# Kernel tuning notes

Hardware: AMD Instinct MI355X
Metric: run time of the kernel (lower is better)

Reference implementation:

```python
import jax, jax.numpy as jnp
import numpy as np

NUM_BINS = 64
BIN_WIDTH = 0.0625
X_SHAPE = (64, 4, 512, 512)  # SD-style latent batch, ~268 MB fp32


def setup_inputs() -> dict:
    key = jax.random.key(0)
    x = jax.random.normal(key, X_SHAPE, dtype=jnp.float32)
    # uniform bin centers over [-2, 2), step = BIN_WIDTH (matches init_kwargs)
    bins = (-2.0 + BIN_WIDTH * jnp.arange(NUM_BINS)).astype(jnp.float32)
    bin_width = jnp.float32(BIN_WIDTH)
    return {"x": x, "bins": bins, "bin_width": bin_width}


def reference(x, bins, bin_width):
    # out[b] = mean(0.5 - 0.5 * tanh((x - bins[b]) / bin_width * 2))
    # lax.map over the small fixed bin axis avoids materializing a
    # [num_bins, *x.shape] intermediate, matching the original's per-bin
    # streaming reduction.
    scale = 2.0 / bin_width

    def per_bin(c):
        return jnp.mean(0.5 - 0.5 * jnp.tanh((x - c) * scale))

    return jax.lax.map(per_bin, bins)  # shape [NUM_BINS]
```

## Files before the change

kernel.cpp:

```cpp
#include <hip/hip_runtime.h>
#include <hip/hip_bf16.h>


#define NCELLS (74 * 64)
#define HIST_BLOCKS 1024
#define HIST_THREADS 256

__global__ void __launch_bounds__(HIST_THREADS)
hist_kernel(const float* __restrict__ x, unsigned* __restrict__ ghist, int n)
{
    __shared__ unsigned hist[NCELLS];
    for (int i = threadIdx.x; i < NCELLS; i += HIST_THREADS) hist[i] = 0u;
    __syncthreads();

    const int n4 = n >> 2;
    const float4* __restrict__ x4 = (const float4*)x;
    const int gid    = blockIdx.x * HIST_THREADS + threadIdx.x;
    const int stride = gridDim.x * HIST_THREADS;

    for (int i = gid; i < n4; i += stride) {
        float4 v = x4[i];
        {
            int f = (int)floorf(fmaf(v.x, 1024.0f, 2368.0f));
            f = min(max(f, 0), NCELLS - 1);
            atomicAdd(&hist[f], 1u);
        }
        {
            int f = (int)floorf(fmaf(v.y, 1024.0f, 2368.0f));
            f = min(max(f, 0), NCELLS - 1);
            atomicAdd(&hist[f], 1u);
        }
        {
            int f = (int)floorf(fmaf(v.z, 1024.0f, 2368.0f));
            f = min(max(f, 0), NCELLS - 1);
            atomicAdd(&hist[f], 1u);
        }
        {
            int f = (int)floorf(fmaf(v.w, 1024.0f, 2368.0f));
            f = min(max(f, 0), NCELLS - 1);
            atomicAdd(&hist[f], 1u);
        }
    }

    if (blockIdx.x == 0) {
        int tail = n & 3;
        if (threadIdx.x < tail) {
            float v = x[n4 * 4 + threadIdx.x];
            int f = (int)floorf(fmaf(v, 1024.0f, 2368.0f));
            f = min(max(f, 0), NCELLS - 1);
            atomicAdd(&hist[f], 1u);
        }
    }

    __syncthreads();
    for (int i = threadIdx.x; i < NCELLS; i += HIST_THREADS) {
        unsigned v = hist[i];
        if (v) atomicAdd(&ghist[i], v);
    }
}

__global__ void __launch_bounds__(256)
bins_kernel(const unsigned* __restrict__ ghist, float* __restrict__ out, float invN)
{
    const int b = blockIdx.x;
    double sum = 0.0;
    for (int f = threadIdx.x; f < NCELLS; f += 256) {
        unsigned h = ghist[f];
        if (h) {
            float t = -5.0f + ((float)f + 0.5f) * (1.0f / 64.0f);
            float z = 4.0f * ((float)b - t);
            float s = 1.0f / (1.0f + __expf(-z));
            sum += (double)h * (double)s;
        }
    }
    __shared__ double sd[256];
    sd[threadIdx.x] = sum;
    __syncthreads();
    for (int ofs = 128; ofs > 0; ofs >>= 1) {
        if (threadIdx.x < ofs) sd[threadIdx.x] += sd[threadIdx.x + ofs];
        __syncthreads();
    }
    if (threadIdx.x == 0) out[b] = (float)(sd[0] * (double)invN);
}

extern "C" void kernel_launch(void* const* d_in, const int* in_sizes, int n_in,
                              void* d_out, int out_size, void* d_ws, size_t ws_size,
                              hipStream_t stream)
{
    const float* x = (const float*)d_in[0];
    const int n = in_sizes[0];
    unsigned* ghist = (unsigned*)d_ws;

    hipMemsetAsync(d_ws, 0, NCELLS * sizeof(unsigned), stream);

    hist_kernel<<<HIST_BLOCKS, HIST_THREADS, 0, stream>>>(x, ghist, n);
    bins_kernel<<<64, 256, 0, stream>>>(ghist, (float*)d_out, 1.0f / (float)n);
}
```

Before: 368.7 us.

## Split histogram atomics between LDS and replicated global copies, window sigmoid

Coarsens the histogram to 32 cells per bin and splits waves so half do LDS atomics and half do global atomics into 256 replicated global histogram copies, spreading atomic contention across both memory paths. A collapse kernel sums the copies, and the final kernel uses the fact that the sigmoid saturates: cells well below a bin count as 1 and only a narrow window gets the sigmoid. This adds a larger memset and an extra kernel launch. Coarser cells and the saturation cutoff change the numerical accuracy of the approximation.

Result: slower. 1.323 ms (+258.8%).

```diff
diff --git a/kernel.cpp b/kernel.cpp
--- a/kernel.cpp
+++ b/kernel.cpp
@@ -2,85 +2,115 @@
 #include <hip/hip_bf16.h>
 
 
-#define NCELLS (74 * 64)
-#define HIST_BLOCKS 1024
-#define HIST_THREADS 256
+#define DLOG   5
+#define MCELLS (74 << DLOG)
+#define NCOPIES 256
+#define HB 2048
+#define HT 256
 
-__global__ void __launch_bounds__(HIST_THREADS)
+__global__ void __launch_bounds__(HT)
 hist_kernel(const float* __restrict__ x, unsigned* __restrict__ ghist, int n)
 {
-    __shared__ unsigned hist[NCELLS];
-    for (int i = threadIdx.x; i < NCELLS; i += HIST_THREADS) hist[i] = 0u;
+    __shared__ unsigned lh[MCELLS];
+    const int tid = threadIdx.x;
+    for (int i = tid; i < MCELLS; i += HT) lh[i] = 0u;
     __syncthreads();
+
+    const int wave = tid >> 6;
+    const bool use_lds = (wave < 2);
+    unsigned* __restrict__ gcopy =
+        ghist + (size_t)((((unsigned)blockIdx.x << 1) | (wave & 1)) & (NCOPIES - 1)) * MCELLS;
 
     const int n4 = n >> 2;
     const float4* __restrict__ x4 = (const float4*)x;
-    const int gid    = blockIdx.x * HIST_THREADS + threadIdx.x;
-    const int stride = gridDim.x * HIST_THREADS;
+    const int stride = HB * (HT * 2);
+    for (int i0 = blockIdx.x * (HT * 2) + tid; i0 < n4; i0 += stride) {
+        const int i1 = i0 + HT;
+        const bool ok1 = (i1 < n4);
+        float4 a = x4[i0];
+        float4 b = ok1 ? x4[i1] : make_float4(0.f, 0.f, 0.f, 0.f);
 
-    for (int i = gid; i < n4; i += stride) {
-        float4 v = x4[i];
-        {
-            int f = (int)floorf(fmaf(v.x, 1024.0f, 2368.0f));
-            f = min(max(f, 0), NCELLS - 1);
-            atomicAdd(&hist[f], 1u);
+        int f0 = min(max((int)floorf(fmaf(a.x, 512.0f, 1184.0f)), 0), MCELLS - 1);
+        int f1 = min(max((int)floorf(fmaf(a.y, 512.0f, 1184.0f)), 0), MCELLS - 1);
+        int f2 = min(max((int)floorf(fmaf(a.z, 512.0f, 1184.0f)), 0), MCELLS - 1);
+        int f3 = min(max((int)floorf(fmaf(a.w, 512.0f, 1184.0f)), 0), MCELLS - 1);
+        if (use_lds) {
+            atomicAdd(&lh[f0], 1u); atomicAdd(&lh[f1], 1u);
+            atomicAdd(&lh[f2], 1u); atomicAdd(&lh[f3], 1u);
+        } else {
+            atomicAdd(&gcopy[f0], 1u); atomicAdd(&gcopy[f1], 1u);
+            atomicAdd(&gcopy[f2], 1u); atomicAdd(&gcopy[f3], 1u);
         }
-        {
-            int f = (int)floorf(fmaf(v.y, 1024.0f, 2368.0f));
-            f = min(max(f, 0), NCELLS - 1);
-            atomicAdd(&hist[f], 1u);
-        }
-        {
-            int f = (int)floorf(fmaf(v.z, 1024.0f, 2368.0f));
-            f = min(max(f, 0), NCELLS - 1);
-            atomicAdd(&hist[f], 1u);
-        }
-        {
-            int f = (int)floorf(fmaf(v.w, 1024.0f, 2368.0f));
-            f = min(max(f, 0), NCELLS - 1);
-            atomicAdd(&hist[f], 1u);
+        if (ok1) {
+            int g0 = min(max((int)floorf(fmaf(b.x, 512.0f, 1184.0f)), 0), MCELLS - 1);
+            int g1 = min(max((int)floorf(fmaf(b.y, 512.0f, 1184.0f)), 0), MCELLS - 1);
+            int g2 = min(max((int)floorf(fmaf(b.z, 512.0f, 1184.0f)), 0), MCELLS - 1);
+            int g3 = min(max((int)floorf(fmaf(b.w, 512.0f, 1184.0f)), 0), MCELLS - 1);
+            if (use_lds) {
+                atomicAdd(&lh[g0], 1u); atomicAdd(&lh[g1], 1u);
+                atomicAdd(&lh[g2], 1u); atomicAdd(&lh[g3], 1u);
+            } else {
+                atomicAdd(&gcopy[g0], 1u); atomicAdd(&gcopy[g1], 1u);
+                atomicAdd(&gcopy[g2], 1u); atomicAdd(&gcopy[g3], 1u);
+            }
         }
     }
-
     if (blockIdx.x == 0) {
         int tail = n & 3;
-        if (threadIdx.x < tail) {
-            float v = x[n4 * 4 + threadIdx.x];
-            int f = (int)floorf(fmaf(v, 1024.0f, 2368.0f));
-            f = min(max(f, 0), NCELLS - 1);
-            atomicAdd(&hist[f], 1u);
+        if (tid < tail) {
+            float v = x[(n >> 2) * 4 + tid];
+            int f = min(max((int)floorf(fmaf(v, 512.0f, 1184.0f)), 0), MCELLS - 1);
+            atomicAdd(&ghist[f], 1u);
         }
     }
+    __syncthreads();
 
-    __syncthreads();
-    for (int i = threadIdx.x; i < NCELLS; i += HIST_THREADS) {
-        unsigned v = hist[i];
-        if (v) atomicAdd(&ghist[i], v);
+    unsigned* __restrict__ fc =
+        ghist + (size_t)(blockIdx.x & (NCOPIES - 1)) * MCELLS;
+    for (int i = tid; i < MCELLS; i += HT) {
+        unsigned v = lh[i];
+        if (v) atomicAdd(&fc[i], v);
     }
 }
 
 __global__ void __launch_bounds__(256)
-bins_kernel(const unsigned* __restrict__ ghist, float* __restrict__ out, float invN)
+collapse_kernel(const unsigned* __restrict__ ghist, unsigned* __restrict__ coll)
 {
-    const int b = blockIdx.x;
-    double sum = 0.0;
-    for (int f = threadIdx.x; f < NCELLS; f += 256) {
-        unsigned h = ghist[f];
-        if (h) {
-            float t = -5.0f + ((float)f + 0.5f) * (1.0f / 64.0f);
-            float z = 4.0f * ((float)b - t);
+    int m = blockIdx.x * 256 + threadIdx.x;
+    if (m >= MCELLS) return;
+    unsigned s = 0;
+    #pragma unroll 8
+    for (int c = 0; c < NCOPIES; ++c) s += ghist[(size_t)c * MCELLS + m];
+    coll[m] = s;
+}
+
+__global__ void __launch_bounds__(256)
+window_kernel(const unsigned* __restrict__ coll, float* __restrict__ out, float invN)
+{
+    const int b   = blockIdx.x;
+    const int tid = threadIdx.x;
+    const int limit = b << DLOG;
+    float acc = 0.0f;
+    for (int m = tid; m < limit; m += 256) acc += (float)coll[m];
+
+    const float zc = 4.0f * (float)b + 19.9375f;
+    #pragma unroll
+    for (int k = 0; k < 2; ++k) {
+        int m = limit + (k << 8) + tid;
+        if (m < limit + (10 << DLOG)) {
+            float z = fmaf((float)m, -0.125f, zc);
             float s = 1.0f / (1.0f + __expf(-z));
-            sum += (double)h * (double)s;
+            acc = fmaf((float)coll[m], s, acc);
         }
     }
     __shared__ double sd[256];
-    sd[threadIdx.x] = sum;
+    sd[tid] = (double)acc;
     __syncthreads();
-    for (int ofs = 128; ofs > 0; ofs >>= 1) {
-        if (threadIdx.x < ofs) sd[threadIdx.x] += sd[threadIdx.x + ofs];
+    for (int o = 128; o > 0; o >>= 1) {
+        if (tid < o) sd[tid] += sd[tid + o];
         __syncthreads();
     }
-    if (threadIdx.x == 0) out[b] = (float)(sd[0] * (double)invN);
+    if (tid == 0) out[b] = (float)(sd[0] * (double)invN);
 }
 
 extern "C" void kernel_launch(void* const* d_in, const int* in_sizes, int n_in,
@@ -90,9 +120,10 @@
     const float* x = (const float*)d_in[0];
     const int n = in_sizes[0];
     unsigned* ghist = (unsigned*)d_ws;
+    unsigned* coll  = ghist + (size_t)NCOPIES * MCELLS;
 
-    hipMemsetAsync(d_ws, 0, NCELLS * sizeof(unsigned), stream);
-
-    hist_kernel<<<HIST_BLOCKS, HIST_THREADS, 0, stream>>>(x, ghist, n);
-    bins_kernel<<<64, 256, 0, stream>>>(ghist, (float*)d_out, 1.0f / (float)n);
+    hipMemsetAsync(ghist, 0, (size_t)NCOPIES * MCELLS * sizeof(unsigned), stream);
+    hist_kernel<<<HB, HT, 0, stream>>>(x, ghist, n);
+    collapse_kernel<<<(MCELLS + 255) / 256, 256, 0, stream>>>(ghist, coll);
+    window_kernel<<<64, 256, 0, stream>>>(coll, (float*)d_out, 1.0f / (float)n);
 }
```
